# Kernel tuning notes

Measured on AMD Instinct MI355X. Metric: run time of the kernel, lower is better.

## Reference

```python
import jax, jax.numpy as jnp
import numpy as np

TEMPERATURE = 0.1
WINDOW = 7  # torch loop: k in range(1, min(8, seq_len - i)) -> offsets 1..7


def _normalize(x, axis=-1, eps=1e-12):
    # F.normalize: x / max(||x||, eps)
    n = jnp.linalg.norm(x, axis=axis, keepdims=True)
    return x / jnp.maximum(n, eps)


def setup_inputs() -> dict:
    key = jax.random.key(0)
    k1, k2 = jax.random.split(key, 2)
    states = jax.random.normal(k1, (4, 16, 1024, 256), dtype=jnp.float32)
    patterns = jax.random.normal(k2, (64, 256), dtype=jnp.float32)
    transfer_weights = jnp.zeros((16, 64, 64), dtype=jnp.float32)
    return {"states": states, "patterns": patterns, "transfer_weights": transfer_weights}


def _forward(states, patterns, transfer_weights):
    b, h, s, d = states.shape
    # --- detect_patterns: similarity to normalized pattern library + softmax ---
    sims = jnp.einsum('bhsd,pd->bhsp', states, _normalize(patterns))
    pattern_scores = jax.nn.softmax(sims / TEMPERATURE, axis=-1)  # [b,h,s,p]

    # --- compute_routing_scores: grad of states.sum() wrt states is ones ->
    #     grad_norm = ||ones||_2 over dim = sqrt(d) (constant), softmax over seq ---
    grad_norm = jnp.full((b, h, s), jnp.sqrt(jnp.float32(d)), dtype=states.dtype)
    routing_scores = jax.nn.softmax(grad_norm / TEMPERATURE, axis=-1)  # uniform [b,h,s]

    # --- optimize_routing: windowed min-plus shortest-path DP ---
    # torch keeps distances [b,h,s,s] but every slice along dim 2 is identical
    # (init and updates only index the last axis), so carry a [b,h,s] vector
    # and broadcast at the end. Pad by WINDOW so near-end updates land in pad.
    inf = jnp.float32(np.inf)
    dist0 = jnp.full((b, h, s + WINDOW), inf, dtype=states.dtype).at[..., 0].set(0.0)
    cost_pad = jnp.pad(-routing_scores, ((0, 0), (0, 0), (0, WINDOW)))

    def step(dist, i):
        cur = jax.lax.dynamic_slice_in_dim(dist, i, 1, axis=-1)          # [b,h,1]
        win = jax.lax.dynamic_slice_in_dim(dist, i + 1, WINDOW, axis=-1)  # [b,h,W]
        c = jax.lax.dynamic_slice_in_dim(cost_pad, i + 1, WINDOW, axis=-1)
        new = jnp.minimum(win, cur + c)
        dist = jax.lax.dynamic_update_slice_in_dim(dist, new, i + 1, axis=-1)
        return dist, None

    dist, _ = jax.lax.scan(step, dist0, jnp.arange(s - 1))
    d_final = dist[..., :s]                                  # [b,h,s]
    optimal_routes = jnp.broadcast_to(d_final[:, :, None, :], (b, h, s, s))

    return routing_scores, optimal_routes, transfer_weights, pattern_scores


def reference(states, patterns, transfer_weights):
    return _forward(states, patterns, transfer_weights)
```

## Files before the change

### kernel.cpp

```cpp
#include <hip/hip_runtime.h>
#include <math.h>

constexpr int B = 4, H = 16, S = 1024, D = 256, P = 64;
constexpr long long N_ROWS = (long long)B * H * S;
constexpr long long OFF_RT = 0;
constexpr long long SZ_RT  = N_ROWS;
constexpr long long OFF_OR = OFF_RT + SZ_RT;
constexpr long long SZ_OR  = N_ROWS * (long long)S;
constexpr long long OFF_TW = OFF_OR + SZ_OR;
constexpr long long SZ_TW  = 16LL * 64 * 64;
constexpr long long OFF_PS = OFF_TW + SZ_TW;

typedef _Float16 half8   __attribute__((ext_vector_type(8)));
typedef _Float16 half4v  __attribute__((ext_vector_type(4)));
typedef float    floatx4 __attribute__((ext_vector_type(4)));

__global__ __launch_bounds__(64) void k_normalize(const float* __restrict__ pat,
                                                  _Float16* __restrict__ pnh,
                                                  _Float16* __restrict__ pnl) {
    int p    = blockIdx.x;
    int lane = threadIdx.x;
    const floatx4* src = (const floatx4*)(pat + (long long)p * D);
    floatx4 v = src[lane];
    float ss = v.x * v.x + v.y * v.y + v.z * v.z + v.w * v.w;
    #pragma unroll
    for (int m = 1; m < 64; m <<= 1) ss += __shfl_xor(ss, m, 64);
    float scale = 10.0f / fmaxf(sqrtf(ss), 1e-12f);
    float a[4] = { v.x * scale, v.y * scale, v.z * scale, v.w * scale };
    half4v hh, ll;
    #pragma unroll
    for (int j = 0; j < 4; ++j) {
        _Float16 h = (_Float16)a[j];
        hh[j] = h;
        ll[j] = (_Float16)(a[j] - (float)h);
    }
    *(half4v*)(pnh + (long long)p * D + lane * 4) = hh;
    *(half4v*)(pnl + (long long)p * D + lane * 4) = ll;
}

__global__ __launch_bounds__(256) void k_small(const floatx4* __restrict__ tw,
                                               float* __restrict__ out) {
    int i = blockIdx.x * 256 + threadIdx.x;
    constexpr int Q = (int)SZ_RT / 4;
    if (i < Q) {
        floatx4 v = { 0.0009765625f, 0.0009765625f, 0.0009765625f, 0.0009765625f };
        ((floatx4*)(out + OFF_RT))[i] = v;
    } else {
        ((floatx4*)(out + OFF_TW))[i - Q] = tw[i - Q];
    }
}

__global__ __launch_bounds__(256) void k_routes(floatx4* __restrict__ out) {
    long long tid = (long long)blockIdx.x * 256 + threadIdx.x;
    int j0 = (int)((tid << 2) & (S - 1));
    float b0 = (float)j0 * (-0.0009765625f);
    floatx4 v;
    v.x = b0;
    v.y = b0 - 0.0009765625f;
    v.z = b0 - 0.001953125f;
    v.w = b0 - 0.0029296875f;
    floatx4* dst = out + tid;
    #pragma unroll
    for (int i = 0; i < 16; ++i) {
        __builtin_nontemporal_store(v, dst + (long long)i * (1 << 20));
    }
}

__global__ __launch_bounds__(256) void k_gemm_mfma(
        const float* __restrict__ states,
        const _Float16* __restrict__ pnh,
        const _Float16* __restrict__ pnl,
        float* __restrict__ out_ps) {
    int wave = threadIdx.x >> 6;
    int lane = threadIdx.x & 63;
    int q    = lane >> 4;
    int m    = lane & 15;
    long long row0 = (long long)blockIdx.x * 64 + wave * 16;
    const float* __restrict__ arow = states + (row0 + m) * D + q * 8;

    floatx4 acc[4] = {floatx4{0,0,0,0}, floatx4{0,0,0,0},
                      floatx4{0,0,0,0}, floatx4{0,0,0,0}};

    #pragma unroll 2
    for (int kk = 0; kk < 8; ++kk) {
        float4 a0 = *(const float4*)(arow + kk * 32);
        float4 a1 = *(const float4*)(arow + kk * 32 + 4);
        float av[8] = { a0.x, a0.y, a0.z, a0.w, a1.x, a1.y, a1.z, a1.w };
        half8 ah, al;
        #pragma unroll
        for (int j = 0; j < 8; ++j) {
            _Float16 h = (_Float16)av[j];
            ah[j] = h;
            al[j] = (_Float16)(av[j] - (float)h);
        }
        #pragma unroll
        for (int t = 0; t < 4; ++t) {
            long long boff = (long long)(t * 16 + m) * D + kk * 32 + q * 8;
            half8 bh = *(const half8*)(pnh + boff);
            half8 bl = *(const half8*)(pnl + boff);
            acc[t] = __builtin_amdgcn_mfma_f32_16x16x32_f16(ah, bh, acc[t], 0, 0, 0);
            acc[t] = __builtin_amdgcn_mfma_f32_16x16x32_f16(al, bh, acc[t], 0, 0, 0);
            acc[t] = __builtin_amdgcn_mfma_f32_16x16x32_f16(ah, bl, acc[t], 0, 0, 0);
        }
    }

    float e[4][4];
    #pragma unroll
    for (int r = 0; r < 4; ++r) {
        float mx = fmaxf(fmaxf(acc[0][r], acc[1][r]), fmaxf(acc[2][r], acc[3][r]));
        #pragma unroll
        for (int msk = 1; msk < 16; msk <<= 1) mx = fmaxf(mx, __shfl_xor(mx, msk, 64));
        float s = 0.0f;
        #pragma unroll
        for (int t = 0; t < 4; ++t) { e[t][r] = __expf(acc[t][r] - mx); s += e[t][r]; }
        #pragma unroll
        for (int msk = 1; msk < 16; msk <<= 1) s += __shfl_xor(s, msk, 64);
        float inv = 1.0f / s;
        long long row = row0 + q * 4 + r;
        #pragma unroll
        for (int t = 0; t < 4; ++t) {
            out_ps[row * P + t * 16 + m] = e[t][r] * inv;
        }
    }
}

extern "C" void kernel_launch(void* const* d_in, const int* in_sizes, int n_in,
                              void* d_out, int out_size, void* d_ws, size_t ws_size,
                              hipStream_t stream) {
    const float* states   = (const float*)d_in[0];
    const float* patterns = (const float*)d_in[1];
    const float* transfer = (const float*)d_in[2];
    float* out = (float*)d_out;
    _Float16* pnh = (_Float16*)d_ws;
    _Float16* pnl = pnh + P * D;

    k_normalize<<<dim3(P), dim3(64), 0, stream>>>(patterns, pnh, pnl);

    k_small<<<dim3(128), dim3(256), 0, stream>>>((const floatx4*)transfer, out);

    k_routes<<<dim3(4096), dim3(256), 0, stream>>>((floatx4*)(out + OFF_OR));

    k_gemm_mfma<<<dim3(1024), dim3(256), 0, stream>>>(states, pnh, pnl, out + OFF_PS);
}
```

Before: 364.1 us.

## Merge route/small fill kernels and split GEMM pattern columns across waves

Folds the small fill kernel (routing scores and transfer-weight copy) and the route-broadcast fill into one launch, with one store per thread and normal stores in place of 16 nontemporal stores. The GEMM now gives each block 32 rows and splits the 64 pattern columns between wave pairs, combining the softmax max and sum through shared memory with two barriers, and doubles the grid. The aim is to cut launch count and raise parallelism in the GEMM. In exchange, each states row is loaded twice across waves, barriers are added, and the nontemporal hint on the 256MB write is dropped, which may change cache behaviour.

```diff
diff --git a/kernel.cpp b/kernel.cpp
--- a/kernel.cpp
+++ b/kernel.cpp
@@ -38,48 +38,53 @@
     *(half4v*)(pnl + (long long)p * D + lane * 4) = ll;
 }
 
-__global__ __launch_bounds__(256) void k_small(const floatx4* __restrict__ tw,
-                                               float* __restrict__ out) {
-    int i = blockIdx.x * 256 + threadIdx.x;
-    constexpr int Q = (int)SZ_RT / 4;
-    if (i < Q) {
-        floatx4 v = { 0.0009765625f, 0.0009765625f, 0.0009765625f, 0.0009765625f };
-        ((floatx4*)(out + OFF_RT))[i] = v;
+__global__ __launch_bounds__(256) void k_routes_small(
+        floatx4* __restrict__ routes,
+        const floatx4* __restrict__ tw,
+        float* __restrict__ out) {
+    long long blk = blockIdx.x;
+    int t = threadIdx.x;
+    if (blk < 65536) {
+        long long i = blk * 256 + t;
+        int j0 = (int)((i << 2) & (S - 1));
+        float b0 = (float)j0 * (-0.0009765625f);
+        floatx4 v;
+        v.x = b0;
+        v.y = b0 - 0.0009765625f;
+        v.z = b0 - 0.001953125f;
+        v.w = b0 - 0.0029296875f;
+        routes[i] = v;
     } else {
-        ((floatx4*)(out + OFF_TW))[i - Q] = tw[i - Q];
+        int i = (int)(blk - 65536) * 256 + t;
+        constexpr int Q = (int)SZ_RT / 4;
+        if (i < Q) {
+            floatx4 v = { 0.0009765625f, 0.0009765625f,
+                          0.0009765625f, 0.0009765625f };
+            ((floatx4*)(out + OFF_RT))[i] = v;
+        } else {
+            ((floatx4*)(out + OFF_TW))[i - Q] = tw[i - Q];
+        }
     }
 }
 
-__global__ __launch_bounds__(256) void k_routes(floatx4* __restrict__ out) {
-    long long tid = (long long)blockIdx.x * 256 + threadIdx.x;
-    int j0 = (int)((tid << 2) & (S - 1));
-    float b0 = (float)j0 * (-0.0009765625f);
-    floatx4 v;
-    v.x = b0;
-    v.y = b0 - 0.0009765625f;
-    v.z = b0 - 0.001953125f;
-    v.w = b0 - 0.0029296875f;
-    floatx4* dst = out + tid;
-    #pragma unroll
-    for (int i = 0; i < 16; ++i) {
-        __builtin_nontemporal_store(v, dst + (long long)i * (1 << 20));
-    }
-}
-
-__global__ __launch_bounds__(256) void k_gemm_mfma(
+__global__ __launch_bounds__(256, 8) void k_gemm_mfma(
         const float* __restrict__ states,
         const _Float16* __restrict__ pnh,
         const _Float16* __restrict__ pnl,
         float* __restrict__ out_ps) {
     int wave = threadIdx.x >> 6;
+    int h    = wave >> 1;
+    int ph   = wave & 1;
     int lane = threadIdx.x & 63;
     int q    = lane >> 4;
     int m    = lane & 15;
-    long long row0 = (long long)blockIdx.x * 64 + wave * 16;
+    long long row0 = (long long)blockIdx.x * 32 + h * 16;
     const float* __restrict__ arow = states + (row0 + m) * D + q * 8;
 
-    floatx4 acc[4] = {floatx4{0,0,0,0}, floatx4{0,0,0,0},
-                      floatx4{0,0,0,0}, floatx4{0,0,0,0}};
+    __shared__ float redmax[2][16][2];
+    __shared__ float redsum[2][16][2];
+
+    floatx4 acc[2] = { floatx4{0,0,0,0}, floatx4{0,0,0,0} };
 
     #pragma unroll 2
     for (int kk = 0; kk < 8; ++kk) {
@@ -89,13 +94,13 @@
         half8 ah, al;
         #pragma unroll
         for (int j = 0; j < 8; ++j) {
-            _Float16 h = (_Float16)av[j];
-            ah[j] = h;
-            al[j] = (_Float16)(av[j] - (float)h);
+            _Float16 hh = (_Float16)av[j];
+            ah[j] = hh;
+            al[j] = (_Float16)(av[j] - (float)hh);
         }
         #pragma unroll
-        for (int t = 0; t < 4; ++t) {
-            long long boff = (long long)(t * 16 + m) * D + kk * 32 + q * 8;
+        for (int t = 0; t < 2; ++t) {
+            long long boff = (long long)(ph * 32 + t * 16 + m) * D + kk * 32 + q * 8;
             half8 bh = *(const half8*)(pnh + boff);
             half8 bl = *(const half8*)(pnl + boff);
             acc[t] = __builtin_amdgcn_mfma_f32_16x16x32_f16(ah, bh, acc[t], 0, 0, 0);
@@ -104,24 +109,44 @@
         }
     }
 
-    float e[4][4];
+    float pmx[4];
     #pragma unroll
     for (int r = 0; r < 4; ++r) {
-        float mx = fmaxf(fmaxf(acc[0][r], acc[1][r]), fmaxf(acc[2][r], acc[3][r]));
+        float mx = fmaxf(acc[0][r], acc[1][r]);
         #pragma unroll
         for (int msk = 1; msk < 16; msk <<= 1) mx = fmaxf(mx, __shfl_xor(mx, msk, 64));
+        pmx[r] = mx;
+        if (m == 0) redmax[h][q * 4 + r][ph] = mx;
+    }
+    __syncthreads();
+
+    float e[2][4];
+    float psum[4];
+    #pragma unroll
+    for (int r = 0; r < 4; ++r) {
+        int rr = q * 4 + r;
+        float gmx = fmaxf(redmax[h][rr][0], redmax[h][rr][1]);
         float s = 0.0f;
         #pragma unroll
-        for (int t = 0; t < 4; ++t) { e[t][r] = __expf(acc[t][r] - mx); s += e[t][r]; }
+        for (int t = 0; t < 2; ++t) { e[t][r] = __expf(acc[t][r] - gmx); s += e[t][r]; }
         #pragma unroll
         for (int msk = 1; msk < 16; msk <<= 1) s += __shfl_xor(s, msk, 64);
-        float inv = 1.0f / s;
-        long long row = row0 + q * 4 + r;
+        psum[r] = s;
+        if (m == 0) redsum[h][rr][ph] = s;
+    }
+    __syncthreads();
+
+    #pragma unroll
+    for (int r = 0; r < 4; ++r) {
+        int rr = q * 4 + r;
+        float inv = 1.0f / (redsum[h][rr][0] + redsum[h][rr][1]);
+        long long row = row0 + rr;
         #pragma unroll
-        for (int t = 0; t < 4; ++t) {
-            out_ps[row * P + t * 16 + m] = e[t][r] * inv;
+        for (int t = 0; t < 2; ++t) {
+            out_ps[row * P + ph * 32 + t * 16 + m] = e[t][r] * inv;
         }
     }
+    (void)pmx; (void)psum;
 }
 
 extern "C" void kernel_launch(void* const* d_in, const int* in_sizes, int n_in,
@@ -136,9 +161,8 @@
 
     k_normalize<<<dim3(P), dim3(64), 0, stream>>>(patterns, pnh, pnl);
 
-    k_small<<<dim3(128), dim3(256), 0, stream>>>((const floatx4*)transfer, out);
+    k_routes_small<<<dim3(65536 + 128), dim3(256), 0, stream>>>(
+        (floatx4*)(out + OFF_OR), (const floatx4*)transfer, out);
 
-    k_routes<<<dim3(4096), dim3(256), 0, stream>>>((floatx4*)(out + OFF_OR));
-
-    k_gemm_mfma<<<dim3(1024), dim3(256), 0, stream>>>(states, pnh, pnl, out + OFF_PS);
+    k_gemm_mfma<<<dim3(2048), dim3(256), 0, stream>>>(states, pnh, pnl, out + OFF_PS);
 }
```

Result: faster. 347.2 us (-4.6%).

## Merge route and small-output kernels, stage GEMM patterns in LDS with prefetch

Applied to the files above, without the earlier changes.

Combines the routes fill and the small-output kernel into a single launch that uses one block per 1024 route elements with regular stores, in place of 16 nontemporal stores per thread. The GEMM kernel now copies the fp16 hi/lo pattern matrices into padded shared memory and reads its B operands from LDS instead of global memory. It also software-prefetches the next A tile from global. The intent is fewer launches and less global B traffic, at the cost of 64K tiny blocks and losing nontemporal stores on the 256MB route write.

```diff
diff --git a/kernel.cpp b/kernel.cpp
--- a/kernel.cpp
+++ b/kernel.cpp
@@ -14,6 +14,8 @@
 typedef _Float16 half8   __attribute__((ext_vector_type(8)));
 typedef _Float16 half4v  __attribute__((ext_vector_type(4)));
 typedef float    floatx4 __attribute__((ext_vector_type(4)));
+
+constexpr int BSTRIDE = 264;
 
 __global__ __launch_bounds__(64) void k_normalize(const float* __restrict__ pat,
                                                   _Float16* __restrict__ pnh,
@@ -38,31 +40,32 @@
     *(half4v*)(pnl + (long long)p * D + lane * 4) = ll;
 }
 
-__global__ __launch_bounds__(256) void k_small(const floatx4* __restrict__ tw,
-                                               float* __restrict__ out) {
-    int i = blockIdx.x * 256 + threadIdx.x;
-    constexpr int Q = (int)SZ_RT / 4;
-    if (i < Q) {
-        floatx4 v = { 0.0009765625f, 0.0009765625f, 0.0009765625f, 0.0009765625f };
-        ((floatx4*)(out + OFF_RT))[i] = v;
+__global__ __launch_bounds__(256) void k_routes_small(
+        floatx4* __restrict__ routes,
+        const floatx4* __restrict__ tw,
+        float* __restrict__ out) {
+    long long blk = blockIdx.x;
+    int t = threadIdx.x;
+    if (blk < 65536) {
+        long long i = blk * 256 + t;
+        int j0 = (int)((i << 2) & (S - 1));
+        float b0 = (float)j0 * (-0.0009765625f);
+        floatx4 v;
+        v.x = b0;
+        v.y = b0 - 0.0009765625f;
+        v.z = b0 - 0.001953125f;
+        v.w = b0 - 0.0029296875f;
+        routes[i] = v;
     } else {
-        ((floatx4*)(out + OFF_TW))[i - Q] = tw[i - Q];
-    }
-}
-
-__global__ __launch_bounds__(256) void k_routes(floatx4* __restrict__ out) {
-    long long tid = (long long)blockIdx.x * 256 + threadIdx.x;
-    int j0 = (int)((tid << 2) & (S - 1));
-    float b0 = (float)j0 * (-0.0009765625f);
-    floatx4 v;
-    v.x = b0;
-    v.y = b0 - 0.0009765625f;
-    v.z = b0 - 0.001953125f;
-    v.w = b0 - 0.0029296875f;
-    floatx4* dst = out + tid;
-    #pragma unroll
-    for (int i = 0; i < 16; ++i) {
-        __builtin_nontemporal_store(v, dst + (long long)i * (1 << 20));
+        int i = (int)(blk - 65536) * 256 + t;
+        constexpr int Q = (int)SZ_RT / 4;
+        if (i < Q) {
+            floatx4 v = { 0.0009765625f, 0.0009765625f,
+                          0.0009765625f, 0.0009765625f };
+            ((floatx4*)(out + OFF_RT))[i] = v;
+        } else {
+            ((floatx4*)(out + OFF_TW))[i - Q] = tw[i - Q];
+        }
     }
 }
 
@@ -71,8 +74,27 @@
         const _Float16* __restrict__ pnh,
         const _Float16* __restrict__ pnl,
         float* __restrict__ out_ps) {
-    int wave = threadIdx.x >> 6;
-    int lane = threadIdx.x & 63;
+    __shared__ _Float16 smem[2 * P * BSTRIDE];
+    _Float16* smH = smem;
+    _Float16* smL = smem + P * BSTRIDE;
+
+    int tid  = threadIdx.x;
+    {
+        const half8* gh = (const half8*)pnh;
+        const half8* gl = (const half8*)pnl;
+        #pragma unroll
+        for (int it = 0; it < 8; ++it) {
+            int idx = it * 256 + tid;
+            int row = idx >> 5;
+            int c8  = idx & 31;
+            *(half8*)&smH[row * BSTRIDE + c8 * 8] = gh[idx];
+            *(half8*)&smL[row * BSTRIDE + c8 * 8] = gl[idx];
+        }
+    }
+    __syncthreads();
+
+    int wave = tid >> 6;
+    int lane = tid & 63;
     int q    = lane >> 4;
     int m    = lane & 15;
     long long row0 = (long long)blockIdx.x * 64 + wave * 16;
@@ -81,10 +103,15 @@
     floatx4 acc[4] = {floatx4{0,0,0,0}, floatx4{0,0,0,0},
                       floatx4{0,0,0,0}, floatx4{0,0,0,0}};
 
-    #pragma unroll 2
+    float4 n0 = *(const float4*)(arow);
+    float4 n1 = *(const float4*)(arow + 4);
+    #pragma unroll
     for (int kk = 0; kk < 8; ++kk) {
-        float4 a0 = *(const float4*)(arow + kk * 32);
-        float4 a1 = *(const float4*)(arow + kk * 32 + 4);
+        float4 a0 = n0, a1 = n1;
+        if (kk < 7) {
+            n0 = *(const float4*)(arow + (kk + 1) * 32);
+            n1 = *(const float4*)(arow + (kk + 1) * 32 + 4);
+        }
         float av[8] = { a0.x, a0.y, a0.z, a0.w, a1.x, a1.y, a1.z, a1.w };
         half8 ah, al;
         #pragma unroll
@@ -95,9 +122,9 @@
         }
         #pragma unroll
         for (int t = 0; t < 4; ++t) {
-            long long boff = (long long)(t * 16 + m) * D + kk * 32 + q * 8;
-            half8 bh = *(const half8*)(pnh + boff);
-            half8 bl = *(const half8*)(pnl + boff);
+            int boff = (t * 16 + m) * BSTRIDE + kk * 32 + q * 8;
+            half8 bh = *(const half8*)&smH[boff];
+            half8 bl = *(const half8*)&smL[boff];
             acc[t] = __builtin_amdgcn_mfma_f32_16x16x32_f16(ah, bh, acc[t], 0, 0, 0);
             acc[t] = __builtin_amdgcn_mfma_f32_16x16x32_f16(al, bh, acc[t], 0, 0, 0);
             acc[t] = __builtin_amdgcn_mfma_f32_16x16x32_f16(ah, bl, acc[t], 0, 0, 0);
@@ -136,9 +163,8 @@
 
     k_normalize<<<dim3(P), dim3(64), 0, stream>>>(patterns, pnh, pnl);
 
-    k_small<<<dim3(128), dim3(256), 0, stream>>>((const floatx4*)transfer, out);
-
-    k_routes<<<dim3(4096), dim3(256), 0, stream>>>((floatx4*)(out + OFF_OR));
+    k_routes_small<<<dim3(65536 + 128), dim3(256), 0, stream>>>(
+        (floatx4*)(out + OFF_OR), (const floatx4*)transfer, out);
 
     k_gemm_mfma<<<dim3(1024), dim3(256), 0, stream>>>(states, pnh, pnl, out + OFF_PS);
 }
```

After: 330.9 us. 9.1% less time.
